# Optimization experiments

Hardware: AMD Instinct MI355X
Metric: run time of the kernel (lower is better)

Reference implementation:

```python
import jax, jax.numpy as jnp
import numpy as np

N, S, Z, H, K, DEG = 8192, 4, 64, 128, 4, 16
E = N * DEG


def setup_inputs() -> dict:
    key = jax.random.key(0)
    ks = jax.random.split(key, 9)
    g = lambda k, shape, scale=1.0: jax.random.normal(k, shape, dtype=jnp.float32) * scale
    return dict(
        zIG=g(ks[0], (N, S, Z)),                         # node intention features
        xt_enc=g(ks[1], (N, S, H)),                      # encoded actions per node
        Ws=g(ks[2], (K, H, Z), 1.0 / np.sqrt(Z)),        # attn_s[k] weights (no bias)
        Wd=g(ks[3], (K, H, Z), 1.0 / np.sqrt(Z)),        # attn_d[k] weights
        F2_w1=g(ks[4], (H, 2 * H), 1.0 / np.sqrt(2 * H)),
        F2_w2=g(ks[5], (H, H), 1.0 / np.sqrt(H)),
        F1_w1=g(ks[6], (H, K * H), 1.0 / np.sqrt(K * H)),
        F1_w2=g(ks[7], (H, H), 1.0 / np.sqrt(H)),
        src=jax.random.randint(ks[8], (E,), 0, N),       # random source per edge
        dst=jnp.repeat(jnp.arange(N), DEG),              # regular graph: DEG in-edges per node, grouped
    )


def reference(zIG, xt_enc, Ws, Wd, F2_w1, F2_w2, F1_w1, F1_w2, src, dst):
    n, s, h = xt_enc.shape
    k = Ws.shape[0]
    deg = src.shape[0] // n

    # ---- edge_attention: eIG[e,s,k] = leaky_relu(sum_h (Ws_k z_src)*(Wd_k z_dst)) ----
    zs, zd = zIG[src], zIG[dst]                          # [E,S,Z] irregular gathers
    scores = []
    for kk in range(k):                                  # k is small & structural
        a_s = zs @ Ws[kk].T                              # [E,S,H]
        a_d = zd @ Wd[kk].T                              # [E,S,H]
        scores.append(jax.nn.leaky_relu((a_s * a_d).sum(-1)))  # [E,S]
    eIG = jnp.stack(scores, axis=-1)                     # [E,S,K]

    # ---- message_func: dA = F2(cat(xt_src, xt_dst)) ----
    msg_in = jnp.concatenate([xt_enc[src], xt_enc[dst]], axis=-1)   # [E,S,2H]
    dA = jax.nn.relu(msg_in @ F2_w1.T) @ F2_w2.T                    # [E,S,H]

    # ---- reduce_func: softmax over neighbor mailbox (dim=1), weighted mean ----
    # dst is grouped with constant degree, so the DGL mailbox is a reshape.
    alpha = jax.nn.softmax(eIG.reshape(n, deg, s, k), axis=1)       # [N,D,S,K]
    mail = dA.reshape(n, deg, s, h)                                 # [N,D,S,H]
    res = jnp.einsum('ndsk,ndsh->nskh', alpha, mail) / deg          # mean over D
    res = res.reshape(n, s, k * h)                                  # cat over k (k-major)
    deltax = jax.nn.relu(res @ F1_w1.T) @ F1_w2.T                   # [N,S,H]
    return deltax, alpha
```

## Files before the change

### kernel.cpp

```cpp
#include <hip/hip_runtime.h>
#include <hip/hip_bf16.h>

typedef unsigned short u16;
typedef unsigned int u32;
using ushort8 = __attribute__((ext_vector_type(8))) unsigned short;
using short8  = __attribute__((ext_vector_type(8))) short;
using f32x4   = __attribute__((ext_vector_type(4))) float;

__device__ __forceinline__ float bf2f(u16 v) {
  union { u32 u; float f; } x; x.u = ((u32)v) << 16; return x.f;
}
__device__ __forceinline__ float u2f(u32 u) {
  union { u32 u; float f; } x; x.u = u; return x.f;
}
__device__ __forceinline__ u16 f2bf(float f) {
  union { u32 u; float f; } x; x.f = f;
  u32 r = x.u + 0x7FFFu + ((x.u >> 16) & 1u);
  return (u16)(r >> 16);
}
__device__ __forceinline__ u32 pack2bf(float lo, float hi) {
  return (u32)f2bf(lo) | ((u32)f2bf(hi) << 16);
}
__device__ __forceinline__ float dot4(float4 a, float4 b) {
  return a.x * b.x + a.y * b.y + a.z * b.z + a.w * b.w;
}
__device__ __forceinline__ void split8(const float* ap, short8& hi, short8& lo) {
  float4 a0 = *(const float4*)ap, a1 = *(const float4*)(ap + 4);
  float e[8] = {a0.x, a0.y, a0.z, a0.w, a1.x, a1.y, a1.z, a1.w};
  u16 h[8], l[8];
  #pragma unroll
  for (int j = 0; j < 8; ++j) {
    u32 b = __float_as_uint(e[j]);
    h[j] = (u16)(b >> 16);
    l[j] = f2bf(e[j] - u2f(b & 0xffff0000u));
  }
  hi = *(short8*)h; lo = *(short8*)l;
}
__device__ __forceinline__ void stage_w(const float* g, int stride, int c, u16* Wl, int t) {
  int row = t >> 1, half = t & 1;
  const float4* gp = (const float4*)(g + (size_t)row * stride + c * 64 + half * 32);
  ushort8* d = (ushort8*)(Wl + row * 72 + half * 32);
  #pragma unroll
  for (int i = 0; i < 4; ++i) {
    float4 a = gp[2 * i], b = gp[2 * i + 1];
    ushort8 o;
    o[0] = f2bf(a.x); o[1] = f2bf(a.y); o[2] = f2bf(a.z); o[3] = f2bf(a.w);
    o[4] = f2bf(b.x); o[5] = f2bf(b.y); o[6] = f2bf(b.z); o[7] = f2bf(b.w);
    d[i] = o;
  }
}

__global__ __launch_bounds__(256) void k_prep(const float* __restrict__ Ws,
                                              const float* __restrict__ Wd,
                                              const float* __restrict__ F1w1,
                                              const float* __restrict__ F2w2,
                                              u16* __restrict__ Bh, u16* __restrict__ Bl,
                                              float* __restrict__ WW2) {
  if (blockIdx.x < 64) {
    int t = blockIdx.x * 256 + threadIdx.x;
    int k = t >> 12, z1 = (t >> 6) & 63, z2 = t & 63;
    const float* wsp = Ws + k * 8192 + z1;
    const float* wdp = Wd + k * 8192 + z2;
    float acc = 0.f;
    #pragma unroll 8
    for (int h = 0; h < 128; ++h) acc += wsp[h * 64] * wdp[h * 64];
    u32 b = __float_as_uint(acc);
    Bh[(k * 64 + z1) * 64 + z2] = (u16)(b >> 16);
    Bl[(k * 64 + z1) * 64 + z2] = f2bf(acc - u2f(b & 0xffff0000u));
  } else {
    int id = (blockIdx.x - 64) * 256 + threadIdx.x;
    int ho = id >> 9, kk = (id >> 7) & 3, hi = id & 127;
    const float* wa = F1w1 + ho * 512 + kk * 128;
    const float* wb = F2w2 + hi;
    float acc = 0.f;
    #pragma unroll 8
    for (int j = 0; j < 128; ++j) acc += wa[j] * wb[j * 128];
    WW2[ho * 512 + kk * 128 + hi] = acc * 0.0625f;
  }
}

__global__ __launch_bounds__(256) void k_td(const float* __restrict__ zIG,
                                            const u16* __restrict__ Bh_g,
                                            const u16* __restrict__ Bl_g,
                                            float* __restrict__ td) {
  __shared__ u16 Bh[128 * 72];
  __shared__ u16 Bl[128 * 72];
  int t = threadIdx.x, lane = t & 63, w = t >> 6;
  int chalf = blockIdx.x & 1;
  size_t rowbase = (size_t)(blockIdx.x >> 1) * 128 + w * 32;
  {
    int row = t >> 1, half = t & 1;
    const ushort8* gh = (const ushort8*)(Bh_g + (chalf * 128 + row) * 64 + half * 32);
    const ushort8* gl = (const ushort8*)(Bl_g + (chalf * 128 + row) * 64 + half * 32);
    ushort8* dh = (ushort8*)(Bh + row * 72 + half * 32);
    ushort8* dl = (ushort8*)(Bl + row * 72 + half * 32);
    #pragma unroll
    for (int i = 0; i < 4; ++i) { dh[i] = gh[i]; dl[i] = gl[i]; }
  }
  __syncthreads();
  int l15 = lane & 15, kc = lane >> 4;
  f32x4 acc[2][8];
  #pragma unroll
  for (int mt = 0; mt < 2; ++mt)
    #pragma unroll
    for (int nt = 0; nt < 8; ++nt) acc[mt][nt] = (f32x4){0.f, 0.f, 0.f, 0.f};
  #pragma unroll
  for (int ks = 0; ks < 2; ++ks) {
    short8 ah[2], al[2];
    #pragma unroll
    for (int mt = 0; mt < 2; ++mt)
      split8(zIG + (rowbase + mt * 16 + l15) * 64 + ks * 32 + kc * 8, ah[mt], al[mt]);
    #pragma unroll
    for (int nt = 0; nt < 8; ++nt) {
      int bo = (nt * 16 + l15) * 72 + ks * 32 + kc * 8;
      short8 bh = *(const short8*)&Bh[bo];
      short8 bl = *(const short8*)&Bl[bo];
      #pragma unroll
      for (int mt = 0; mt < 2; ++mt) {
        acc[mt][nt] = __builtin_amdgcn_mfma_f32_16x16x32_bf16(ah[mt], bh, acc[mt][nt], 0, 0, 0);
        acc[mt][nt] = __builtin_amdgcn_mfma_f32_16x16x32_bf16(al[mt], bh, acc[mt][nt], 0, 0, 0);
        acc[mt][nt] = __builtin_amdgcn_mfma_f32_16x16x32_bf16(ah[mt], bl, acc[mt][nt], 0, 0, 0);
      }
    }
  }
  #pragma unroll
  for (int mt = 0; mt < 2; ++mt)
    #pragma unroll
    for (int nt = 0; nt < 8; ++nt)
      #pragma unroll
      for (int j = 0; j < 4; ++j)
        td[(rowbase + mt * 16 + kc * 4 + j) * 256 + chalf * 128 + nt * 16 + l15] =
            acc[mt][nt][j];
}

__global__ __launch_bounds__(256) void k_uv(const float* __restrict__ xt,
                                            const float* __restrict__ W1,
                                            u16* __restrict__ u, u16* __restrict__ v) {
  __shared__ u16 Wlu[128 * 72];
  __shared__ u16 Wlv[128 * 72];
  int t = threadIdx.x, lane = t & 63, w = t >> 6;
  size_t rowbase = (size_t)blockIdx.x * 128 + w * 32;
  int l15 = lane & 15, kc = lane >> 4;
  f32x4 au[2][8], av[2][8];
  #pragma unroll
  for (int mt = 0; mt < 2; ++mt)
    #pragma unroll
    for (int nt = 0; nt < 8; ++nt) {
      au[mt][nt] = (f32x4){0.f, 0.f, 0.f, 0.f};
      av[mt][nt] = (f32x4){0.f, 0.f, 0.f, 0.f};
    }
  for (int c = 0; c < 2; ++c) {
    __syncthreads();
    stage_w(W1,       256, c, Wlu, t);
    stage_w(W1 + 128, 256, c, Wlv, t);
    __syncthreads();
    #pragma unroll
    for (int ks = 0; ks < 2; ++ks) {
      short8 af[2];
      #pragma unroll
      for (int mt = 0; mt < 2; ++mt) {
        const float* ap = xt + (rowbase + mt * 16 + l15) * 128 + c * 64 + ks * 32 + kc * 8;
        float4 a0 = *(const float4*)ap, a1 = *(const float4*)(ap + 4);
        u16 tmp[8] = {f2bf(a0.x), f2bf(a0.y), f2bf(a0.z), f2bf(a0.w),
                      f2bf(a1.x), f2bf(a1.y), f2bf(a1.z), f2bf(a1.w)};
        af[mt] = *(short8*)tmp;
      }
      #pragma unroll
      for (int nt = 0; nt < 8; ++nt) {
        short8 bu = *(const short8*)&Wlu[(nt * 16 + l15) * 72 + ks * 32 + kc * 8];
        short8 bv = *(const short8*)&Wlv[(nt * 16 + l15) * 72 + ks * 32 + kc * 8];
        #pragma unroll
        for (int mt = 0; mt < 2; ++mt) {
          au[mt][nt] = __builtin_amdgcn_mfma_f32_16x16x32_bf16(af[mt], bu, au[mt][nt], 0, 0, 0);
          av[mt][nt] = __builtin_amdgcn_mfma_f32_16x16x32_bf16(af[mt], bv, av[mt][nt], 0, 0, 0);
        }
      }
    }
  }
  #pragma unroll
  for (int mt = 0; mt < 2; ++mt)
    #pragma unroll
    for (int nt = 0; nt < 8; ++nt)
      #pragma unroll
      for (int j = 0; j < 4; ++j) {
        size_t idx = (rowbase + mt * 16 + kc * 4 + j) * 128 + nt * 16 + l15;
        u[idx] = f2bf(au[mt][nt][j]);
        v[idx] = f2bf(av[mt][nt][j]);
      }
}

__global__ __launch_bounds__(256) void k_score(
    const float* __restrict__ zIG, const int* __restrict__ src,
    const float* __restrict__ td, const u16* __restrict__ uW, const u16* __restrict__ vW,
    float* __restrict__ out, u16* __restrict__ m_ws) {
  __shared__ int srcIdx[16];
  __shared__ float tds[16 * 68];
  __shared__ float s17[16 * 17];
  __shared__ float e17[16 * 17];
  __shared__ float a20[16 * 20];

  int t = threadIdx.x, n = blockIdx.x;
  if (t < 16) srcIdx[t] = src[n * 16 + t];
  {
    int r = t >> 4, cc = t & 15;
    *(float4*)&tds[r * 68 + cc * 4] = ((const float4*)(td + (size_t)n * 1024))[r * 16 + cc];
  }
  __syncthreads();
  {
    int d = t >> 4, s = (t >> 2) & 3, k = t & 3;
    int sn = srcIdx[d];
    const float4* zp = (const float4*)(zIG + (size_t)sn * 256 + s * 64);
    int base = s * 4;
    float p0 = 0.f, p1 = 0.f, p2 = 0.f, p3 = 0.f;
    #pragma unroll
    for (int i = 0; i < 4; ++i) {
      float4 zv = zp[i * 4 + k];
      int o = i * 16 + k * 4;
      p0 += dot4(zv, *(const float4*)&tds[(base + 0) * 68 + o]);
      p1 += dot4(zv, *(const float4*)&tds[(base + 1) * 68 + o]);
      p2 += dot4(zv, *(const float4*)&tds[(base + 2) * 68 + o]);
      p3 += dot4(zv, *(const float4*)&tds[(base + 3) * 68 + o]);
    }
    p0 += __shfl_xor(p0, 1); p1 += __shfl_xor(p1, 1);
    p2 += __shfl_xor(p2, 1); p3 += __shfl_xor(p3, 1);
    p0 += __shfl_xor(p0, 2); p1 += __shfl_xor(p1, 2);
    p2 += __shfl_xor(p2, 2); p3 += __shfl_xor(p3, 2);
    float acc = (k == 0) ? p0 : (k == 1) ? p1 : (k == 2) ? p2 : p3;
    s17[d * 17 + base + k] = acc > 0.f ? acc : 0.01f * acc;
  }
  __syncthreads();
  float e_own;
  int dC = t >> 4, skC = t & 15;
  {
    float mx = -3.4e38f;
    #pragma unroll
    for (int dd = 0; dd < 16; ++dd) mx = fmaxf(mx, s17[dd * 17 + skC]);
    e_own = __expf(s17[dC * 17 + skC] - mx);
    e17[dC * 17 + skC] = e_own;
  }
  __syncthreads();
  {
    float sum = 0.f;
    #pragma unroll
    for (int dd = 0; dd < 16; ++dd) sum += e17[dd * 17 + skC];
    float a = e_own / sum;
    a20[dC * 20 + skC] = a;
    out[4194304u + (unsigned)n * 256 + t] = a;
  }
  __syncthreads();
  {
    int hp = t & 63, s = t >> 6;
    u32 vbits = *(const u32*)(vW + (size_t)n * 512 + s * 128 + hp * 2);
    float v_lo = u2f(vbits << 16), v_hi = u2f(vbits & 0xffff0000u);
    const u32* up = (const u32*)uW;
    float m0l = 0.f, m0h = 0.f, m1l = 0.f, m1h = 0.f;
    float m2l = 0.f, m2h = 0.f, m3l = 0.f, m3h = 0.f;
    for (int d = 0; d < 16; ++d) {
      int sn = srcIdx[d];
      u32 ub = up[(size_t)sn * 256 + s * 64 + hp];
      float r_lo = fmaxf(u2f(ub << 16) + v_lo, 0.f);
      float r_hi = fmaxf(u2f(ub & 0xffff0000u) + v_hi, 0.f);
      float4 a = *(const float4*)&a20[d * 20 + s * 4];
      m0l += a.x * r_lo; m0h += a.x * r_hi;
      m1l += a.y * r_lo; m1h += a.y * r_hi;
      m2l += a.z * r_lo; m2h += a.z * r_hi;
      m3l += a.w * r_lo; m3h += a.w * r_hi;
    }
    u32* mp = (u32*)(m_ws + (size_t)n * 2048);
    mp[(s * 4 + 0) * 64 + hp] = pack2bf(m0l, m0h);
    mp[(s * 4 + 1) * 64 + hp] = pack2bf(m1l, m1h);
    mp[(s * 4 + 2) * 64 + hp] = pack2bf(m2l, m2h);
    mp[(s * 4 + 3) * 64 + hp] = pack2bf(m3l, m3h);
  }
}

__global__ __launch_bounds__(256) void k_fg(const u16* __restrict__ A,
                                            const float* __restrict__ WF,
                                            const float* __restrict__ WG,
                                            float* __restrict__ out) {
  __shared__ u16 Wl[128 * 72];
  __shared__ u16 hidl[128 * 136];
  int t = threadIdx.x, lane = t & 63, w = t >> 6;
  size_t rowbase = (size_t)blockIdx.x * 128 + w * 32;
  int l15 = lane & 15, kc = lane >> 4;
  f32x4 acc[2][8];
  #pragma unroll
  for (int mt = 0; mt < 2; ++mt)
    #pragma unroll
    for (int nt = 0; nt < 8; ++nt) acc[mt][nt] = (f32x4){0.f, 0.f, 0.f, 0.f};
  for (int c = 0; c < 8; ++c) {
    __syncthreads();
    stage_w(WF, 512, c, Wl, t);
    __syncthreads();
    #pragma unroll
    for (int ks = 0; ks < 2; ++ks) {
      short8 af[2];
      #pragma unroll
      for (int mt = 0; mt < 2; ++mt)
        af[mt] = *(const short8*)(A + (rowbase + mt * 16 + l15) * 512 + c * 64 + ks * 32 + kc * 8);
      #pragma unroll
      for (int nt = 0; nt < 8; ++nt) {
        short8 bf = *(const short8*)&Wl[(nt * 16 + l15) * 72 + ks * 32 + kc * 8];
        #pragma unroll
        for (int mt = 0; mt < 2; ++mt)
          acc[mt][nt] = __builtin_amdgcn_mfma_f32_16x16x32_bf16(af[mt], bf, acc[mt][nt], 0, 0, 0);
      }
    }
  }
  #pragma unroll
  for (int mt = 0; mt < 2; ++mt)
    #pragma unroll
    for (int nt = 0; nt < 8; ++nt)
      #pragma unroll
      for (int j = 0; j < 4; ++j)
        hidl[(w * 32 + mt * 16 + kc * 4 + j) * 136 + nt * 16 + l15] =
            f2bf(fmaxf(acc[mt][nt][j], 0.f));
  f32x4 acc2[2][8];
  #pragma unroll
  for (int mt = 0; mt < 2; ++mt)
    #pragma unroll
    for (int nt = 0; nt < 8; ++nt) acc2[mt][nt] = (f32x4){0.f, 0.f, 0.f, 0.f};
  for (int c = 0; c < 2; ++c) {
    __syncthreads();
    stage_w(WG, 128, c, Wl, t);
    __syncthreads();
    #pragma unroll
    for (int ks = 0; ks < 2; ++ks) {
      short8 af[2];
      #pragma unroll
      for (int mt = 0; mt < 2; ++mt)
        af[mt] = *(const short8*)&hidl[(w * 32 + mt * 16 + l15) * 136 + c * 64 + ks * 32 + kc * 8];
      #pragma unroll
      for (int nt = 0; nt < 8; ++nt) {
        short8 bf = *(const short8*)&Wl[(nt * 16 + l15) * 72 + ks * 32 + kc * 8];
        #pragma unroll
        for (int mt = 0; mt < 2; ++mt)
          acc2[mt][nt] = __builtin_amdgcn_mfma_f32_16x16x32_bf16(af[mt], bf, acc2[mt][nt], 0, 0, 0);
      }
    }
  }
  #pragma unroll
  for (int mt = 0; mt < 2; ++mt)
    #pragma unroll
    for (int nt = 0; nt < 8; ++nt)
      #pragma unroll
      for (int j = 0; j < 4; ++j)
        out[(rowbase + mt * 16 + kc * 4 + j) * 128 + nt * 16 + l15] = acc2[mt][nt][j];
}

extern "C" void kernel_launch(void* const* d_in, const int* in_sizes, int n_in,
                              void* d_out, int out_size, void* d_ws, size_t ws_size,
                              hipStream_t stream) {
  const float* zIG  = (const float*)d_in[0];
  const float* xt   = (const float*)d_in[1];
  const float* Ws   = (const float*)d_in[2];
  const float* Wd   = (const float*)d_in[3];
  const float* F2w1 = (const float*)d_in[4];
  const float* F2w2 = (const float*)d_in[5];
  const float* F1w1 = (const float*)d_in[6];
  const float* F1w2 = (const float*)d_in[7];
  const int* src    = (const int*)d_in[8];
  float* out = (float*)d_out;

  char* ws = (char*)d_ws;
  u16* Bh    = (u16*)ws;
  u16* Bl    = Bh + 16384;
  float* td  = (float*)(ws + 65536);
  u16* u     = (u16*)(ws + 65536 + 33554432);
  u16* v     = u + 4194304;
  float* WW2 = (float*)(ws + 50397184);
  u16* m     = (u16*)(ws + 50659328);

  k_prep <<<320,  256, 0, stream>>>(Ws, Wd, F1w1, F2w2, Bh, Bl, WW2);
  k_td   <<<512,  256, 0, stream>>>(zIG, Bh, Bl, td);
  k_uv   <<<256,  256, 0, stream>>>(xt, F2w1, u, v);
  k_score<<<8192, 256, 0, stream>>>(zIG, src, td, u, v, out, m);
  k_fg   <<<256,  256, 0, stream>>>(m, WW2, F1w2, out);
}
```

Before: 106.2 us.

## Merge td/uv kernels, process two nodes per score block, widen fg blocks

```diff
diff --git a/kernel.cpp b/kernel.cpp
--- a/kernel.cpp
+++ b/kernel.cpp
@@ -42,6 +42,19 @@
   ushort8* d = (ushort8*)(Wl + row * 72 + half * 32);
   #pragma unroll
   for (int i = 0; i < 4; ++i) {
+    float4 a = gp[2 * i], b = gp[2 * i + 1];
+    ushort8 o;
+    o[0] = f2bf(a.x); o[1] = f2bf(a.y); o[2] = f2bf(a.z); o[3] = f2bf(a.w);
+    o[4] = f2bf(b.x); o[5] = f2bf(b.y); o[6] = f2bf(b.z); o[7] = f2bf(b.w);
+    d[i] = o;
+  }
+}
+__device__ __forceinline__ void stage_w512(const float* g, int stride, int c, u16* Wl, int t) {
+  int row = t >> 2, q = t & 3;
+  const float4* gp = (const float4*)(g + (size_t)row * stride + c * 64 + q * 16);
+  ushort8* d = (ushort8*)(Wl + row * 72 + q * 16);
+  #pragma unroll
+  for (int i = 0; i < 2; ++i) {
     float4 a = gp[2 * i], b = gp[2 * i + 1];
     ushort8 o;
     o[0] = f2bf(a.x); o[1] = f2bf(a.y); o[2] = f2bf(a.z); o[3] = f2bf(a.w);
@@ -79,273 +92,279 @@
   }
 }
 
-__global__ __launch_bounds__(256) void k_td(const float* __restrict__ zIG,
-                                            const u16* __restrict__ Bh_g,
-                                            const u16* __restrict__ Bl_g,
-                                            float* __restrict__ td) {
-  __shared__ u16 Bh[128 * 72];
-  __shared__ u16 Bl[128 * 72];
+__global__ __launch_bounds__(256) void k_tduv(const float* __restrict__ zIG,
+                                              const u16* __restrict__ Bh_g,
+                                              const u16* __restrict__ Bl_g,
+                                              const float* __restrict__ xt,
+                                              const float* __restrict__ W1,
+                                              float* __restrict__ td,
+                                              u16* __restrict__ u, u16* __restrict__ v) {
+  __shared__ __align__(16) u16 WlA[128 * 72];
+  __shared__ __align__(16) u16 WlB[128 * 72];
   int t = threadIdx.x, lane = t & 63, w = t >> 6;
-  int chalf = blockIdx.x & 1;
-  size_t rowbase = (size_t)(blockIdx.x >> 1) * 128 + w * 32;
-  {
-    int row = t >> 1, half = t & 1;
-    const ushort8* gh = (const ushort8*)(Bh_g + (chalf * 128 + row) * 64 + half * 32);
-    const ushort8* gl = (const ushort8*)(Bl_g + (chalf * 128 + row) * 64 + half * 32);
-    ushort8* dh = (ushort8*)(Bh + row * 72 + half * 32);
-    ushort8* dl = (ushort8*)(Bl + row * 72 + half * 32);
-    #pragma unroll
-    for (int i = 0; i < 4; ++i) { dh[i] = gh[i]; dl[i] = gl[i]; }
-  }
-  __syncthreads();
   int l15 = lane & 15, kc = lane >> 4;
-  f32x4 acc[2][8];
-  #pragma unroll
-  for (int mt = 0; mt < 2; ++mt)
-    #pragma unroll
-    for (int nt = 0; nt < 8; ++nt) acc[mt][nt] = (f32x4){0.f, 0.f, 0.f, 0.f};
-  #pragma unroll
-  for (int ks = 0; ks < 2; ++ks) {
-    short8 ah[2], al[2];
+  if (blockIdx.x < 512) {
+    u16* Bh = WlA;
+    u16* Bl = WlB;
+    int chalf = blockIdx.x & 1;
+    size_t rowbase = (size_t)(blockIdx.x >> 1) * 128 + w * 32;
+    {
+      int row = t >> 1, half = t & 1;
+      const ushort8* gh = (const ushort8*)(Bh_g + (chalf * 128 + row) * 64 + half * 32);
+      const ushort8* gl = (const ushort8*)(Bl_g + (chalf * 128 + row) * 64 + half * 32);
+      ushort8* dh = (ushort8*)(Bh + row * 72 + half * 32);
+      ushort8* dl = (ushort8*)(Bl + row * 72 + half * 32);
+      #pragma unroll
+      for (int i = 0; i < 4; ++i) { dh[i] = gh[i]; dl[i] = gl[i]; }
+    }
+    __syncthreads();
+    f32x4 acc[2][8];
     #pragma unroll
     for (int mt = 0; mt < 2; ++mt)
-      split8(zIG + (rowbase + mt * 16 + l15) * 64 + ks * 32 + kc * 8, ah[mt], al[mt]);
-    #pragma unroll
-    for (int nt = 0; nt < 8; ++nt) {
-      int bo = (nt * 16 + l15) * 72 + ks * 32 + kc * 8;
-      short8 bh = *(const short8*)&Bh[bo];
-      short8 bl = *(const short8*)&Bl[bo];
-      #pragma unroll
-      for (int mt = 0; mt < 2; ++mt) {
-        acc[mt][nt] = __builtin_amdgcn_mfma_f32_16x16x32_bf16(ah[mt], bh, acc[mt][nt], 0, 0, 0);
-        acc[mt][nt] = __builtin_amdgcn_mfma_f32_16x16x32_bf16(al[mt], bh, acc[mt][nt], 0, 0, 0);
-        acc[mt][nt] = __builtin_amdgcn_mfma_f32_16x16x32_bf16(ah[mt], bl, acc[mt][nt], 0, 0, 0);
-      }
-    }
-  }
-  #pragma unroll
-  for (int mt = 0; mt < 2; ++mt)
-    #pragma unroll
-    for (int nt = 0; nt < 8; ++nt)
-      #pragma unroll
-      for (int j = 0; j < 4; ++j)
-        td[(rowbase + mt * 16 + kc * 4 + j) * 256 + chalf * 128 + nt * 16 + l15] =
-            acc[mt][nt][j];
-}
-
-__global__ __launch_bounds__(256) void k_uv(const float* __restrict__ xt,
-                                            const float* __restrict__ W1,
-                                            u16* __restrict__ u, u16* __restrict__ v) {
-  __shared__ u16 Wlu[128 * 72];
-  __shared__ u16 Wlv[128 * 72];
-  int t = threadIdx.x, lane = t & 63, w = t >> 6;
-  size_t rowbase = (size_t)blockIdx.x * 128 + w * 32;
-  int l15 = lane & 15, kc = lane >> 4;
-  f32x4 au[2][8], av[2][8];
-  #pragma unroll
-  for (int mt = 0; mt < 2; ++mt)
-    #pragma unroll
-    for (int nt = 0; nt < 8; ++nt) {
-      au[mt][nt] = (f32x4){0.f, 0.f, 0.f, 0.f};
-      av[mt][nt] = (f32x4){0.f, 0.f, 0.f, 0.f};
-    }
-  for (int c = 0; c < 2; ++c) {
-    __syncthreads();
-    stage_w(W1,       256, c, Wlu, t);
-    stage_w(W1 + 128, 256, c, Wlv, t);
-    __syncthreads();
+      #pragma unroll
+      for (int nt = 0; nt < 8; ++nt) acc[mt][nt] = (f32x4){0.f, 0.f, 0.f, 0.f};
     #pragma unroll
     for (int ks = 0; ks < 2; ++ks) {
-      short8 af[2];
-      #pragma unroll
-      for (int mt = 0; mt < 2; ++mt) {
-        const float* ap = xt + (rowbase + mt * 16 + l15) * 128 + c * 64 + ks * 32 + kc * 8;
-        float4 a0 = *(const float4*)ap, a1 = *(const float4*)(ap + 4);
-        u16 tmp[8] = {f2bf(a0.x), f2bf(a0.y), f2bf(a0.z), f2bf(a0.w),
-                      f2bf(a1.x), f2bf(a1.y), f2bf(a1.z), f2bf(a1.w)};
-        af[mt] = *(short8*)tmp;
-      }
+      short8 ah[2], al[2];
+      #pragma unroll
+      for (int mt = 0; mt < 2; ++mt)
+        split8(zIG + (rowbase + mt * 16 + l15) * 64 + ks * 32 + kc * 8, ah[mt], al[mt]);
       #pragma unroll
       for (int nt = 0; nt < 8; ++nt) {
-        short8 bu = *(const short8*)&Wlu[(nt * 16 + l15) * 72 + ks * 32 + kc * 8];
-        short8 bv = *(const short8*)&Wlv[(nt * 16 + l15) * 72 + ks * 32 + kc * 8];
+        int bo = (nt * 16 + l15) * 72 + ks * 32 + kc * 8;
+        short8 bh = *(const short8*)&Bh[bo];
+        short8 bl = *(const short8*)&Bl[bo];
         #pragma unroll
         for (int mt = 0; mt < 2; ++mt) {
-          au[mt][nt] = __builtin_amdgcn_mfma_f32_16x16x32_bf16(af[mt], bu, au[mt][nt], 0, 0, 0);
-          av[mt][nt] = __builtin_amdgcn_mfma_f32_16x16x32_bf16(af[mt], bv, av[mt][nt], 0, 0, 0);
+          acc[mt][nt] = __builtin_amdgcn_mfma_f32_16x16x32_bf16(ah[mt], bh, acc[mt][nt], 0, 0, 0);
+          acc[mt][nt] = __builtin_amdgcn_mfma_f32_16x16x32_bf16(al[mt], bh, acc[mt][nt], 0, 0, 0);
+          acc[mt][nt] = __builtin_amdgcn_mfma_f32_16x16x32_bf16(ah[mt], bl, acc[mt][nt], 0, 0, 0);
         }
       }
     }
-  }
-  #pragma unroll
-  for (int mt = 0; mt < 2; ++mt)
-    #pragma unroll
-    for (int nt = 0; nt < 8; ++nt)
-      #pragma unroll
-      for (int j = 0; j < 4; ++j) {
-        size_t idx = (rowbase + mt * 16 + kc * 4 + j) * 128 + nt * 16 + l15;
-        u[idx] = f2bf(au[mt][nt][j]);
-        v[idx] = f2bf(av[mt][nt][j]);
-      }
+    #pragma unroll
+    for (int mt = 0; mt < 2; ++mt)
+      #pragma unroll
+      for (int nt = 0; nt < 8; ++nt)
+        #pragma unroll
+        for (int j = 0; j < 4; ++j)
+          td[(rowbase + mt * 16 + kc * 4 + j) * 256 + chalf * 128 + nt * 16 + l15] =
+              acc[mt][nt][j];
+  } else {
+    u16* Wlu = WlA;
+    u16* Wlv = WlB;
+    size_t rowbase = (size_t)(blockIdx.x - 512) * 128 + w * 32;
+    f32x4 au[2][8], av[2][8];
+    #pragma unroll
+    for (int mt = 0; mt < 2; ++mt)
+      #pragma unroll
+      for (int nt = 0; nt < 8; ++nt) {
+        au[mt][nt] = (f32x4){0.f, 0.f, 0.f, 0.f};
+        av[mt][nt] = (f32x4){0.f, 0.f, 0.f, 0.f};
+      }
+    for (int c = 0; c < 2; ++c) {
+      __syncthreads();
+      stage_w(W1,       256, c, Wlu, t);
+      stage_w(W1 + 128, 256, c, Wlv, t);
+      __syncthreads();
+      #pragma unroll
+      for (int ks = 0; ks < 2; ++ks) {
+        short8 af[2];
+        #pragma unroll
+        for (int mt = 0; mt < 2; ++mt) {
+          const float* ap = xt + (rowbase + mt * 16 + l15) * 128 + c * 64 + ks * 32 + kc * 8;
+          float4 a0 = *(const float4*)ap, a1 = *(const float4*)(ap + 4);
+          u16 tmp[8] = {f2bf(a0.x), f2bf(a0.y), f2bf(a0.z), f2bf(a0.w),
+                        f2bf(a1.x), f2bf(a1.y), f2bf(a1.z), f2bf(a1.w)};
+          af[mt] = *(short8*)tmp;
+        }
+        #pragma unroll
+        for (int nt = 0; nt < 8; ++nt) {
+          short8 bu = *(const short8*)&Wlu[(nt * 16 + l15) * 72 + ks * 32 + kc * 8];
+          short8 bv = *(const short8*)&Wlv[(nt * 16 + l15) * 72 + ks * 32 + kc * 8];
+          #pragma unroll
+          for (int mt = 0; mt < 2; ++mt) {
+            au[mt][nt] = __builtin_amdgcn_mfma_f32_16x16x32_bf16(af[mt], bu, au[mt][nt], 0, 0, 0);
+            av[mt][nt] = __builtin_amdgcn_mfma_f32_16x16x32_bf16(af[mt], bv, av[mt][nt], 0, 0, 0);
+          }
+        }
+      }
+    }
+    #pragma unroll
+    for (int mt = 0; mt < 2; ++mt)
+      #pragma unroll
+      for (int nt = 0; nt < 8; ++nt)
+        #pragma unroll
+        for (int j = 0; j < 4; ++j) {
+          size_t idx = (rowbase + mt * 16 + kc * 4 + j) * 128 + nt * 16 + l15;
+          u[idx] = f2bf(au[mt][nt][j]);
+          v[idx] = f2bf(av[mt][nt][j]);
+        }
+  }
 }
 
 __global__ __launch_bounds__(256) void k_score(
     const float* __restrict__ zIG, const int* __restrict__ src,
     const float* __restrict__ td, const u16* __restrict__ uW, const u16* __restrict__ vW,
     float* __restrict__ out, u16* __restrict__ m_ws) {
-  __shared__ int srcIdx[16];
-  __shared__ float tds[16 * 68];
-  __shared__ float s17[16 * 17];
-  __shared__ float e17[16 * 17];
-  __shared__ float a20[16 * 20];
-
-  int t = threadIdx.x, n = blockIdx.x;
-  if (t < 16) srcIdx[t] = src[n * 16 + t];
-  {
-    int r = t >> 4, cc = t & 15;
-    *(float4*)&tds[r * 68 + cc * 4] = ((const float4*)(td + (size_t)n * 1024))[r * 16 + cc];
+  __shared__ int srcIdx[32];
+  __shared__ float tds[2][16 * 68];
+  __shared__ float s17[2][16 * 17];
+  __shared__ float e17[2][16 * 17];
+  __shared__ float a20[2][16 * 20];
+
+  int t = threadIdx.x, n0 = blockIdx.x * 2;
+  if (t < 32) srcIdx[t] = src[n0 * 16 + t];
+  #pragma unroll
+  for (int i = 0; i < 2; ++i) {
+    int idx = t + i * 256;
+    int nd = idx >> 8, r = (idx >> 4) & 15, cc = idx & 15;
+    *(float4*)&tds[nd][r * 68 + cc * 4] =
+        ((const float4*)td)[(size_t)(n0 + nd) * 256 + r * 16 + cc];
   }
   __syncthreads();
   {
     int d = t >> 4, s = (t >> 2) & 3, k = t & 3;
-    int sn = srcIdx[d];
-    const float4* zp = (const float4*)(zIG + (size_t)sn * 256 + s * 64);
     int base = s * 4;
-    float p0 = 0.f, p1 = 0.f, p2 = 0.f, p3 = 0.f;
-    #pragma unroll
-    for (int i = 0; i < 4; ++i) {
-      float4 zv = zp[i * 4 + k];
-      int o = i * 16 + k * 4;
-      p0 += dot4(zv, *(const float4*)&tds[(base + 0) * 68 + o]);
-      p1 += dot4(zv, *(const float4*)&tds[(base + 1) * 68 + o]);
-      p2 += dot4(zv, *(const float4*)&tds[(base + 2) * 68 + o]);
-      p3 += dot4(zv, *(const float4*)&tds[(base + 3) * 68 + o]);
-    }
-    p0 += __shfl_xor(p0, 1); p1 += __shfl_xor(p1, 1);
-    p2 += __shfl_xor(p2, 1); p3 += __shfl_xor(p3, 1);
-    p0 += __shfl_xor(p0, 2); p1 += __shfl_xor(p1, 2);
-    p2 += __shfl_xor(p2, 2); p3 += __shfl_xor(p3, 2);
-    float acc = (k == 0) ? p0 : (k == 1) ? p1 : (k == 2) ? p2 : p3;
-    s17[d * 17 + base + k] = acc > 0.f ? acc : 0.01f * acc;
+    float4 zr[2][4];
+    #pragma unroll
+    for (int nd = 0; nd < 2; ++nd) {
+      int sn = srcIdx[nd * 16 + d];
+      const float4* zp = (const float4*)(zIG + (size_t)sn * 256 + s * 64);
+      #pragma unroll
+      for (int i = 0; i < 4; ++i) zr[nd][i] = zp[i * 4 + k];
+    }
+    #pragma unroll
+    for (int nd = 0; nd < 2; ++nd) {
+      float p0 = 0.f, p1 = 0.f, p2 = 0.f, p3 = 0.f;
+      #pragma unroll
+      for (int i = 0; i < 4; ++i) {
+        float4 zv = zr[nd][i];
+        int o = i * 16 + k * 4;
+        p0 += dot4(zv, *(const float4*)&tds[nd][(base + 0) * 68 + o]);
+        p1 += dot4(zv, *(const float4*)&tds[nd][(base + 1) * 68 + o]);
+        p2 += dot4(zv, *(const float4*)&tds[nd][(base + 2) * 68 + o]);
+        p3 += dot4(zv, *(const float4*)&tds[nd][(base + 3) * 68 + o]);
+      }
+      p0 += __shfl_xor(p0, 1); p1 += __shfl_xor(p1, 1);
+      p2 += __shfl_xor(p2, 1); p3 += __shfl_xor(p3, 1);
+      p0 += __shfl_xor(p0, 2); p1 += __shfl_xor(p1, 2);
+      p2 += __shfl_xor(p2, 2); p3 += __shfl_xor(p3, 2);
+      float acc = (k == 0) ? p0 : (k == 1) ? p1 : (k == 2) ? p2 : p3;
+      s17[nd][d * 17 + base + k] = acc > 0.f ? acc : 0.01f * acc;
+    }
+  }
+  int hp = t & 63, sD = t >> 6;
+  u32 upre[2][16], vbits[2];
+  {
+    const u32* up = (const u32*)uW;
+    #pragma unroll
+    for (int nd = 0; nd < 2; ++nd) {
+      #pragma unroll
+      for (int dd = 0; dd < 16; ++dd)
+        upre[nd][dd] = up[(size_t)srcIdx[nd * 16 + dd] * 256 + sD * 64 + hp];
+      vbits[nd] = *(const u32*)(vW + (size_t)(n0 + nd) * 512 + sD * 128 + hp * 2);
+    }
   }
   __syncthreads();
-  float e_own;
+  float e_own[2];
   int dC = t >> 4, skC = t & 15;
-  {
+  #pragma unroll
+  for (int nd = 0; nd < 2; ++nd) {
     float mx = -3.4e38f;
     #pragma unroll
-    for (int dd = 0; dd < 16; ++dd) mx = fmaxf(mx, s17[dd * 17 + skC]);
-    e_own = __expf(s17[dC * 17 + skC] - mx);
-    e17[dC * 17 + skC] = e_own;
+    for (int dd = 0; dd < 16; ++dd) mx = fmaxf(mx, s17[nd][dd * 17 + skC]);
+    e_own[nd] = __expf(s17[nd][dC * 17 + skC] - mx);
+    e17[nd][dC * 17 + skC] = e_own[nd];
   }
   __syncthreads();
-  {
+  #pragma unroll
+  for (int nd = 0; nd < 2; ++nd) {
     float sum = 0.f;
     #pragma unroll
-    for (int dd = 0; dd < 16; ++dd) sum += e17[dd * 17 + skC];
-    float a = e_own / sum;
-    a20[dC * 20 + skC] = a;
-    out[4194304u + (unsigned)n * 256 + t] = a;
+    for (int dd = 0; dd < 16; ++dd) sum += e17[nd][dd * 17 + skC];
+    float a = e_own[nd] / sum;
+    a20[nd][dC * 20 + skC] = a;
+    out[4194304u + (unsigned)(n0 + nd) * 256 + t] = a;
   }
   __syncthreads();
-  {
-    int hp = t & 63, s = t >> 6;
-    u32 vbits = *(const u32*)(vW + (size_t)n * 512 + s * 128 + hp * 2);
-    float v_lo = u2f(vbits << 16), v_hi = u2f(vbits & 0xffff0000u);
-    const u32* up = (const u32*)uW;
+  #pragma unroll
+  for (int nd = 0; nd < 2; ++nd) {
+    float v_lo = u2f(vbits[nd] << 16), v_hi = u2f(vbits[nd] & 0xffff0000u);
     float m0l = 0.f, m0h = 0.f, m1l = 0.f, m1h = 0.f;
     float m2l = 0.f, m2h = 0.f, m3l = 0.f, m3h = 0.f;
-    for (int d = 0; d < 16; ++d) {
-      int sn = srcIdx[d];
-      u32 ub = up[(size_t)sn * 256 + s * 64 + hp];
+    #pragma unroll
+    for (int dd = 0; dd < 16; ++dd) {
+      u32 ub = upre[nd][dd];
       float r_lo = fmaxf(u2f(ub << 16) + v_lo, 0.f);
       float r_hi = fmaxf(u2f(ub & 0xffff0000u) + v_hi, 0.f);
-      float4 a = *(const float4*)&a20[d * 20 + s * 4];
+      float4 a = *(const float4*)&a20[nd][dd * 20 + sD * 4];
       m0l += a.x * r_lo; m0h += a.x * r_hi;
       m1l += a.y * r_lo; m1h += a.y * r_hi;
       m2l += a.z * r_lo; m2h += a.z * r_hi;
       m3l += a.w * r_lo; m3h += a.w * r_hi;
     }
-    u32* mp = (u32*)(m_ws + (size_t)n * 2048);
-    mp[(s * 4 + 0) * 64 + hp] = pack2bf(m0l, m0h);
-    mp[(s * 4 + 1) * 64 + hp] = pack2bf(m1l, m1h);
-    mp[(s * 4 + 2) * 64 + hp] = pack2bf(m2l, m2h);
-    mp[(s * 4 + 3) * 64 + hp] = pack2bf(m3l, m3h);
-  }
-}
-
-__global__ __launch_bounds__(256) void k_fg(const u16* __restrict__ A,
+    u32* mp = (u32*)(m_ws + (size_t)(n0 + nd) * 2048);
+    mp[(sD * 4 + 0) * 64 + hp] = pack2bf(m0l, m0h);
+    mp[(sD * 4 + 1) * 64 + hp] = pack2bf(m1l, m1h);
+    mp[(sD * 4 + 2) * 64 + hp] = pack2bf(m2l, m2h);
+    mp[(sD * 4 + 3) * 64 + hp] = pack2bf(m3l, m3h);
+  }
+}
+
+__global__ __launch_bounds__(512) void k_fg(const u16* __restrict__ A,
                                             const float* __restrict__ WF,
                                             const float* __restrict__ WG,
                                             float* __restrict__ out) {
   __shared__ u16 Wl[128 * 72];
   __shared__ u16 hidl[128 * 136];
   int t = threadIdx.x, lane = t & 63, w = t >> 6;
-  size_t rowbase = (size_t)blockIdx.x * 128 + w * 32;
+  size_t rowbase = (size_t)blockIdx.x * 128 + w * 16;
   int l15 = lane & 15, kc = lane >> 4;
-  f32x4 acc[2][8];
-  #pragma unroll
-  for (int mt = 0; mt < 2; ++mt)
-    #pragma unroll
-    for (int nt = 0; nt < 8; ++nt) acc[mt][nt] = (f32x4){0.f, 0.f, 0.f, 0.f};
+  f32x4 acc[8];
+  #pragma unroll
+  for (int nt = 0; nt < 8; ++nt) acc[nt] = (f32x4){0.f, 0.f, 0.f, 0.f};
   for (int c = 0; c < 8; ++c) {
     __syncthreads();
-    stage_w(WF, 512, c, Wl, t);
+    stage_w512(WF, 512, c, Wl, t);
     __syncthreads();
     #pragma unroll
     for (int ks = 0; ks < 2; ++ks) {
-      short8 af[2];
-      #pragma unroll
-      for (int mt = 0; mt < 2; ++mt)
-        af[mt] = *(const short8*)(A + (rowbase + mt * 16 + l15) * 512 + c * 64 + ks * 32 + kc * 8);
+      short8 af = *(const short8*)(A + (rowbase + l15) * 512 + c * 64 + ks * 32 + kc * 8);
       #pragma unroll
       for (int nt = 0; nt < 8; ++nt) {
         short8 bf = *(const short8*)&Wl[(nt * 16 + l15) * 72 + ks * 32 + kc * 8];
-        #pragma unroll
-        for (int mt = 0; mt < 2; ++mt)
-          acc[mt][nt] = __builtin_amdgcn_mfma_f32_16x16x32_bf16(af[mt], bf, acc[mt][nt], 0, 0, 0);
-      }
-    }
-  }
-  #pragma unroll
-  for (int mt = 0; mt < 2; ++mt)
-    #pragma unroll
-    for (int nt = 0; nt < 8; ++nt)
-      #pragma unroll
-      for (int j = 0; j < 4; ++j)
-        hidl[(w * 32 + mt * 16 + kc * 4 + j) * 136 + nt * 16 + l15] =
-            f2bf(fmaxf(acc[mt][nt][j], 0.f));
-  f32x4 acc2[2][8];
-  #pragma unroll
-  for (int mt = 0; mt < 2; ++mt)
-    #pragma unroll
-    for (int nt = 0; nt < 8; ++nt) acc2[mt][nt] = (f32x4){0.f, 0.f, 0.f, 0.f};
+        acc[nt] = __builtin_amdgcn_mfma_f32_16x16x32_bf16(af, bf, acc[nt], 0, 0, 0);
+      }
+    }
+  }
+  #pragma unroll
+  for (int nt = 0; nt < 8; ++nt)
+    #pragma unroll
+    for (int j = 0; j < 4; ++j)
+      hidl[(w * 16 + kc * 4 + j) * 136 + nt * 16 + l15] = f2bf(fmaxf(acc[nt][j], 0.f));
+  f32x4 acc2[8];
+  #pragma unroll
+  for (int nt = 0; nt < 8; ++nt) acc2[nt] = (f32x4){0.f, 0.f, 0.f, 0.f};
   for (int c = 0; c < 2; ++c) {
     __syncthreads();
-    stage_w(WG, 128, c, Wl, t);
+    stage_w512(WG, 128, c, Wl, t);
     __syncthreads();
     #pragma unroll
     for (int ks = 0; ks < 2; ++ks) {
-      short8 af[2];
-      #pragma unroll
-      for (int mt = 0; mt < 2; ++mt)
-        af[mt] = *(const short8*)&hidl[(w * 32 + mt * 16 + l15) * 136 + c * 64 + ks * 32 + kc * 8];
+      short8 af = *(const short8*)&hidl[(w * 16 + l15) * 136 + c * 64 + ks * 32 + kc * 8];
       #pragma unroll
       for (int nt = 0; nt < 8; ++nt) {
         short8 bf = *(const short8*)&Wl[(nt * 16 + l15) * 72 + ks * 32 + kc * 8];
-        #pragma unroll
-        for (int mt = 0; mt < 2; ++mt)
-          acc2[mt][nt] = __builtin_amdgcn_mfma_f32_16x16x32_bf16(af[mt], bf, acc2[mt][nt], 0, 0, 0);
-      }
-    }
-  }
-  #pragma unroll
-  for (int mt = 0; mt < 2; ++mt)
-    #pragma unroll
-    for (int nt = 0; nt < 8; ++nt)
-      #pragma unroll
-      for (int j = 0; j < 4; ++j)
-        out[(rowbase + mt * 16 + kc * 4 + j) * 128 + nt * 16 + l15] = acc2[mt][nt][j];
+        acc2[nt] = __builtin_amdgcn_mfma_f32_16x16x32_bf16(af, bf, acc2[nt], 0, 0, 0);
+      }
+    }
+  }
+  #pragma unroll
+  for (int nt = 0; nt < 8; ++nt)
+    #pragma unroll
+    for (int j = 0; j < 4; ++j)
+      out[(rowbase + kc * 4 + j) * 128 + nt * 16 + l15] = acc2[nt][j];
 }
 
 extern "C" void kernel_launch(void* const* d_in, const int* in_sizes, int n_in,
@@ -372,8 +391,7 @@
   u16* m     = (u16*)(ws + 50659328);
 
   k_prep <<<320,  256, 0, stream>>>(Ws, Wd, F1w1, F2w2, Bh, Bl, WW2);
-  k_td   <<<512,  256, 0, stream>>>(zIG, Bh, Bl, td);
-  k_uv   <<<256,  256, 0, stream>>>(xt, F2w1, u, v);
-  k_score<<<8192, 256, 0, stream>>>(zIG, src, td, u, v, out, m);
-  k_fg   <<<256,  256, 0, stream>>>(m, WW2, F1w2, out);
-}
+  k_tduv <<<768,  256, 0, stream>>>(zIG, Bh, Bl, xt, F2w1, td, u, v);
+  k_score<<<4096, 256, 0, stream>>>(zIG, src, td, u, v, out, m);
+  k_fg   <<<256,  512, 0, stream>>>(m, WW2, F1w2, out);
+}
```

Result: faster. 101.4 us (-4.5%).
